# Optimization experiments

Measured on AMD Instinct MI355X. Metric: run time of the kernel, lower is better.

## Reference

```python
import jax, jax.numpy as jnp
import numpy as np

B, N, D = 4096, 64, 128
H, ATT = 8, 32
SCALE = ATT ** -0.5


def setup_inputs() -> dict:
    key = jax.random.key(0)
    k1, k2, k3, k4, k5 = jax.random.split(key, 5)
    x = jax.random.normal(k1, (B, N, D), dtype=jnp.float32)
    # glorot-ish scale for weights
    W_Q = jax.random.normal(k2, (H, D, ATT), dtype=jnp.float32) * (2.0 / (D + ATT)) ** 0.5
    W_K = jax.random.normal(k3, (H, D, ATT), dtype=jnp.float32) * (2.0 / (D + ATT)) ** 0.5
    W_V = jax.random.normal(k4, (H, D, ATT), dtype=jnp.float32) * (2.0 / (D + ATT)) ** 0.5
    W_res = jax.random.normal(k5, (D, H * ATT), dtype=jnp.float32) * (2.0 / (D + H * ATT)) ** 0.5
    return {"x": x, "W_Q": W_Q, "W_K": W_K, "W_V": W_V, "W_res": W_res}


def reference(x, W_Q, W_K, W_V, W_res):
    # per-head projections: (B,N,D) x (H,D,K) -> (B,H,N,K)
    Q = jnp.einsum('bnd,hdk->bhnk', x, W_Q)
    K = jnp.einsum('bnd,hdk->bhnk', x, W_K)
    V = jnp.einsum('bnd,hdk->bhnk', x, W_V)
    scores = jnp.einsum('bhnk,bhmk->bhnm', Q, K) * SCALE  # (B,H,N,N)
    attn = jax.nn.softmax(scores, axis=-1)
    ctx = jnp.einsum('bhnm,bhmk->bhnk', attn, V)          # (B,H,N,K)
    ctx = ctx.transpose(0, 2, 1, 3).reshape(x.shape[0], x.shape[1], H * ATT)
    res = x @ W_res  # d != H*att_dim -> residual projection
    return jax.nn.relu(ctx + res)
```

## Files before the change

### kernel.cpp

```cpp
#include <hip/hip_runtime.h>

#define NB    4096
#define SEQ   64
#define DIM   128
#define NHEAD 8
#define ATTD  32
#define HKC   256
#define SCALE 0.17677669529663687f
#define LOG2E 1.4426950408889634f

typedef __bf16 bf16_t;
typedef __bf16 bf16x8 __attribute__((ext_vector_type(8)));
typedef __bf16 bf16x4 __attribute__((ext_vector_type(4)));
typedef float  f32x4  __attribute__((ext_vector_type(4)));
typedef short  s16x4  __attribute__((ext_vector_type(4)));
typedef unsigned int u32;

#define MFMA16(a, b, c) __builtin_amdgcn_mfma_f32_16x16x16bf16_1k(a, b, c, 0, 0, 0)

static __device__ __forceinline__ u32 pkbf(float a, float b) {
  unsigned short ua = __builtin_bit_cast(unsigned short, (__bf16)a);
  unsigned short ub = __builtin_bit_cast(unsigned short, (__bf16)b);
  return (u32)ua | ((u32)ub << 16);
}

static __device__ __forceinline__ s16x4 pk4(f32x4 t) {
  union { u32 u[2]; s16x4 s; } r;
  r.u[0] = pkbf(t[0], t[1]);
  r.u[1] = pkbf(t[2], t[3]);
  return r.s;
}

#define XSWZ(r, c) (((r) << 7) + ((c) ^ (((r) & 7) << 3)))

__global__ void prep_weights(const float* __restrict__ Wq,
                             const float* __restrict__ Wk,
                             const float* __restrict__ Wv,
                             const float* __restrict__ Wr,
                             bf16_t* __restrict__ ws) {
  int idx = blockIdx.x * 256 + threadIdx.x;
  int m = idx >> 15;
  int e = idx & 32767;
  int c = e >> 7;
  int d = e & 127;
  float v;
  if (m == 0)      v = Wq[((c >> 5) * DIM + d) * ATTD + (c & 31)] * (SCALE * LOG2E);
  else if (m == 1) v = Wk[((c >> 5) * DIM + d) * ATTD + (c & 31)];
  else if (m == 2) v = Wv[((c >> 5) * DIM + d) * ATTD + (c & 31)];
  else             v = Wr[d * HKC + c];
  ws[idx] = (bf16_t)v;
}

__launch_bounds__(256, 3)
__global__ void fused_attn(const float* __restrict__ xg,
                           const bf16_t* __restrict__ ws,
                           float* __restrict__ outg) {
  __shared__ bf16_t Xb[64 * 128];

  const int t  = threadIdx.x;
  const int w  = t >> 6;
  const int l  = t & 63;
  const int lo = l & 15;
  const int g  = l >> 4;
  const int b  = blockIdx.x;

  {
    const float* xb = xg + (size_t)b * (SEQ * DIM);
#pragma unroll
    for (int i = 0; i < 8; ++i) {
      int idx = i * 1024 + t * 4;
      float4 v = *(const float4*)(xb + idx);
      bf16x4 p;
      p[0] = (bf16_t)v.x; p[1] = (bf16_t)v.y; p[2] = (bf16_t)v.z; p[3] = (bf16_t)v.w;
      *(bf16x4*)&Xb[XSWZ(idx >> 7, idx & 127)] = p;
    }
  }
  __syncthreads();

  const bf16_t* wsq = ws;
  const bf16_t* wsk = ws + 32768;
  const bf16_t* wsv = ws + 65536;
  const bf16_t* wsr = ws + 98304;
  float* ob = outg + (size_t)b * (SEQ * HKC);
  const f32x4 z4 = {0.f, 0.f, 0.f, 0.f};

#pragma unroll
  for (int hh = 0; hh < 2; ++hh) {
    const int hc = w * 64 + hh * 32;

    s16x4 kfr[2][4], vfr[4][2], qfr[2][4];

    {
      f32x4 acck[2][4];
#pragma unroll
      for (int i = 0; i < 2; ++i)
#pragma unroll
        for (int j = 0; j < 4; ++j) acck[i][j] = z4;
#pragma unroll
      for (int kk = 0; kk < 4; ++kk) {
        bf16x8 aw[2], bx[4];
#pragma unroll
        for (int at = 0; at < 2; ++at)
          aw[at] = *(const bf16x8*)(wsk + (hc + at * 16 + lo) * DIM + kk * 32 + g * 8);
#pragma unroll
        for (int nt = 0; nt < 4; ++nt)
          bx[nt] = *(const bf16x8*)&Xb[XSWZ(nt * 16 + lo, kk * 32 + g * 8)];
        __builtin_amdgcn_s_setprio(1);
#pragma unroll
        for (int at = 0; at < 2; ++at)
#pragma unroll
          for (int nt = 0; nt < 4; ++nt)
            acck[at][nt] = __builtin_amdgcn_mfma_f32_16x16x32_bf16(aw[at], bx[nt], acck[at][nt], 0, 0, 0);
        __builtin_amdgcn_s_setprio(0);
      }
#pragma unroll
      for (int at = 0; at < 2; ++at)
#pragma unroll
        for (int nt = 0; nt < 4; ++nt) kfr[at][nt] = pk4(acck[at][nt]);
    }

    {
      f32x4 accv[4][2];
#pragma unroll
      for (int i = 0; i < 4; ++i)
#pragma unroll
        for (int j = 0; j < 2; ++j) accv[i][j] = z4;
#pragma unroll
      for (int kk = 0; kk < 4; ++kk) {
        bf16x8 ax[4], bw[2];
#pragma unroll
        for (int nt = 0; nt < 4; ++nt)
          ax[nt] = *(const bf16x8*)&Xb[XSWZ(nt * 16 + lo, kk * 32 + g * 8)];
#pragma unroll
        for (int ct = 0; ct < 2; ++ct)
          bw[ct] = *(const bf16x8*)(wsv + (hc + ct * 16 + lo) * DIM + kk * 32 + g * 8);
        __builtin_amdgcn_s_setprio(1);
#pragma unroll
        for (int nt = 0; nt < 4; ++nt)
#pragma unroll
          for (int ct = 0; ct < 2; ++ct)
            accv[nt][ct] = __builtin_amdgcn_mfma_f32_16x16x32_bf16(ax[nt], bw[ct], accv[nt][ct], 0, 0, 0);
        __builtin_amdgcn_s_setprio(0);
      }
#pragma unroll
      for (int nt = 0; nt < 4; ++nt)
#pragma unroll
        for (int ct = 0; ct < 2; ++ct) vfr[nt][ct] = pk4(accv[nt][ct]);
    }

    {
      f32x4 accq[2][4];
#pragma unroll
      for (int i = 0; i < 2; ++i)
#pragma unroll
        for (int j = 0; j < 4; ++j) accq[i][j] = z4;
#pragma unroll
      for (int kk = 0; kk < 4; ++kk) {
        bf16x8 aw[2], bx[4];
#pragma unroll
        for (int at = 0; at < 2; ++at)
          aw[at] = *(const bf16x8*)(wsq + (hc + at * 16 + lo) * DIM + kk * 32 + g * 8);
#pragma unroll
        for (int mt = 0; mt < 4; ++mt)
          bx[mt] = *(const bf16x8*)&Xb[XSWZ(mt * 16 + lo, kk * 32 + g * 8)];
        __builtin_amdgcn_s_setprio(1);
#pragma unroll
        for (int at = 0; at < 2; ++at)
#pragma unroll
          for (int mt = 0; mt < 4; ++mt)
            accq[at][mt] = __builtin_amdgcn_mfma_f32_16x16x32_bf16(aw[at], bx[mt], accq[at][mt], 0, 0, 0);
        __builtin_amdgcn_s_setprio(0);
      }
#pragma unroll
      for (int at = 0; at < 2; ++at)
#pragma unroll
        for (int mt = 0; mt < 4; ++mt) qfr[at][mt] = pk4(accq[at][mt]);
    }

    f32x4 ch[2][4];
#pragma unroll
    for (int i = 0; i < 2; ++i)
#pragma unroll
      for (int j = 0; j < 4; ++j) ch[i][j] = z4;
#pragma unroll
    for (int mt = 0; mt < 4; ++mt) {
      f32x4 sv[4];
      __builtin_amdgcn_s_setprio(1);
#pragma unroll
      for (int nt = 0; nt < 4; ++nt)
        sv[nt] = MFMA16(kfr[0][nt], qfr[0][mt], z4);
#pragma unroll
      for (int nt = 0; nt < 4; ++nt)
        sv[nt] = MFMA16(kfr[1][nt], qfr[1][mt], sv[nt]);
      __builtin_amdgcn_s_setprio(0);
      bf16x8 bxr[4], awr[2];
#pragma unroll
      for (int mtj = 0; mtj < 4; ++mtj)
        bxr[mtj] = *(const bf16x8*)&Xb[XSWZ(mtj * 16 + lo, mt * 32 + g * 8)];
#pragma unroll
      for (int ct = 0; ct < 2; ++ct)
        awr[ct] = *(const bf16x8*)(wsr + (hc + ct * 16 + lo) * DIM + mt * 32 + g * 8);
      float ps[4];
#pragma unroll
      for (int nt = 0; nt < 4; ++nt) {
        float e0 = __builtin_amdgcn_exp2f(sv[nt][0]);
        float e1 = __builtin_amdgcn_exp2f(sv[nt][1]);
        float e2 = __builtin_amdgcn_exp2f(sv[nt][2]);
        float e3 = __builtin_amdgcn_exp2f(sv[nt][3]);
        sv[nt][0] = e0; sv[nt][1] = e1; sv[nt][2] = e2; sv[nt][3] = e3;
        ps[nt] = (e0 + e1) + (e2 + e3);
      }
      float sum = (ps[0] + ps[1]) + (ps[2] + ps[3]);
      s16x4 pfr[4];
#pragma unroll
      for (int nt = 0; nt < 4; ++nt) pfr[nt] = pk4(sv[nt]);
      __builtin_amdgcn_s_setprio(1);
#pragma unroll
      for (int ct = 0; ct < 2; ++ct)
#pragma unroll
        for (int mtj = 0; mtj < 4; ++mtj)
          ch[ct][mtj] = __builtin_amdgcn_mfma_f32_16x16x32_bf16(awr[ct], bxr[mtj], ch[ct][mtj], 0, 0, 0);
      __builtin_amdgcn_s_setprio(0);
      sum += __shfl_xor(sum, 16, 64);
      sum += __shfl_xor(sum, 32, 64);
      float rinv = __builtin_amdgcn_rcpf(sum);
      __builtin_amdgcn_s_setprio(1);
#pragma unroll
      for (int ct = 0; ct < 2; ++ct) {
        f32x4 a = MFMA16(vfr[0][ct], pfr[0], z4);
        a = MFMA16(vfr[1][ct], pfr[1], a);
        a = MFMA16(vfr[2][ct], pfr[2], a);
        a = MFMA16(vfr[3][ct], pfr[3], a);
#pragma unroll
        for (int j = 0; j < 4; ++j)
          ch[ct][mt][j] = fmaf(a[j], rinv, ch[ct][mt][j]);
      }
      __builtin_amdgcn_s_setprio(0);
    }

#pragma unroll
    for (int ct = 0; ct < 2; ++ct)
#pragma unroll
      for (int mt = 0; mt < 4; ++mt) {
        float4 o;
        o.x = fmaxf(ch[ct][mt][0], 0.f);
        o.y = fmaxf(ch[ct][mt][1], 0.f);
        o.z = fmaxf(ch[ct][mt][2], 0.f);
        o.w = fmaxf(ch[ct][mt][3], 0.f);
        *(float4*)(ob + (mt * 16 + lo) * HKC + hc + ct * 16 + 4 * g) = o;
      }
  }
}

extern "C" void kernel_launch(void* const* d_in, const int* in_sizes, int n_in,
                              void* d_out, int out_size, void* d_ws, size_t ws_size,
                              hipStream_t stream) {
  const float* x  = (const float*)d_in[0];
  const float* Wq = (const float*)d_in[1];
  const float* Wk = (const float*)d_in[2];
  const float* Wv = (const float*)d_in[3];
  const float* Wr = (const float*)d_in[4];
  bf16_t* ws = (bf16_t*)d_ws;
  float* out = (float*)d_out;

  prep_weights<<<512, 256, 0, stream>>>(Wq, Wk, Wv, Wr, ws);
  fused_attn<<<NB, 256, 0, stream>>>(x, ws, out);
}
```

Baseline: 178.3 us.

## Compute residual per query tile and store immediately to cut registers

The residual projection is restructured so each query tile computes its own 16-row residual block over the full K dimension, instead of accumulating all four tiles across the softmax loop. Each tile's output is written right after its attention step, so the eight persistent accumulators shrink to two. Launch bounds rise from 3 to 4 blocks per SIMD to use the freed registers for occupancy. The MFMA count is unchanged, but the global weight and LDS loads inside the loop are reorganized, and spills are possible if the new register cap is too tight.

```diff
diff --git a/kernel.cpp b/kernel.cpp
--- a/kernel.cpp
+++ b/kernel.cpp
@@ -51,7 +51,7 @@
   ws[idx] = (bf16_t)v;
 }
 
-__launch_bounds__(256, 3)
+__launch_bounds__(256, 4)
 __global__ void fused_attn(const float* __restrict__ xg,
                            const bf16_t* __restrict__ ws,
                            float* __restrict__ outg) {
@@ -177,11 +177,6 @@
         for (int mt = 0; mt < 4; ++mt) qfr[at][mt] = pk4(accq[at][mt]);
     }
 
-    f32x4 ch[2][4];
-#pragma unroll
-    for (int i = 0; i < 2; ++i)
-#pragma unroll
-      for (int j = 0; j < 4; ++j) ch[i][j] = z4;
 #pragma unroll
     for (int mt = 0; mt < 4; ++mt) {
       f32x4 sv[4];
@@ -193,13 +188,6 @@
       for (int nt = 0; nt < 4; ++nt)
         sv[nt] = MFMA16(kfr[1][nt], qfr[1][mt], sv[nt]);
       __builtin_amdgcn_s_setprio(0);
-      bf16x8 bxr[4], awr[2];
-#pragma unroll
-      for (int mtj = 0; mtj < 4; ++mtj)
-        bxr[mtj] = *(const bf16x8*)&Xb[XSWZ(mtj * 16 + lo, mt * 32 + g * 8)];
-#pragma unroll
-      for (int ct = 0; ct < 2; ++ct)
-        awr[ct] = *(const bf16x8*)(wsr + (hc + ct * 16 + lo) * DIM + mt * 32 + g * 8);
       float ps[4];
 #pragma unroll
       for (int nt = 0; nt < 4; ++nt) {
@@ -214,13 +202,17 @@
       s16x4 pfr[4];
 #pragma unroll
       for (int nt = 0; nt < 4; ++nt) pfr[nt] = pk4(sv[nt]);
-      __builtin_amdgcn_s_setprio(1);
-#pragma unroll
-      for (int ct = 0; ct < 2; ++ct)
-#pragma unroll
-        for (int mtj = 0; mtj < 4; ++mtj)
-          ch[ct][mtj] = __builtin_amdgcn_mfma_f32_16x16x32_bf16(awr[ct], bxr[mtj], ch[ct][mtj], 0, 0, 0);
-      __builtin_amdgcn_s_setprio(0);
+      f32x4 ch[2] = {z4, z4};
+#pragma unroll
+      for (int kk = 0; kk < 4; ++kk) {
+        bf16x8 bxr = *(const bf16x8*)&Xb[XSWZ(mt * 16 + lo, kk * 32 + g * 8)];
+        bf16x8 awr0 = *(const bf16x8*)(wsr + (hc + lo) * DIM + kk * 32 + g * 8);
+        bf16x8 awr1 = *(const bf16x8*)(wsr + (hc + 16 + lo) * DIM + kk * 32 + g * 8);
+        __builtin_amdgcn_s_setprio(1);
+        ch[0] = __builtin_amdgcn_mfma_f32_16x16x32_bf16(awr0, bxr, ch[0], 0, 0, 0);
+        ch[1] = __builtin_amdgcn_mfma_f32_16x16x32_bf16(awr1, bxr, ch[1], 0, 0, 0);
+        __builtin_amdgcn_s_setprio(0);
+      }
       sum += __shfl_xor(sum, 16, 64);
       sum += __shfl_xor(sum, 32, 64);
       float rinv = __builtin_amdgcn_rcpf(sum);
@@ -233,22 +225,19 @@
         a = MFMA16(vfr[3][ct], pfr[3], a);
 #pragma unroll
         for (int j = 0; j < 4; ++j)
-          ch[ct][mt][j] = fmaf(a[j], rinv, ch[ct][mt][j]);
+          ch[ct][j] = fmaf(a[j], rinv, ch[ct][j]);
       }
       __builtin_amdgcn_s_setprio(0);
-    }
-
-#pragma unroll
-    for (int ct = 0; ct < 2; ++ct)
-#pragma unroll
-      for (int mt = 0; mt < 4; ++mt) {
+#pragma unroll
+      for (int ct = 0; ct < 2; ++ct) {
         float4 o;
-        o.x = fmaxf(ch[ct][mt][0], 0.f);
-        o.y = fmaxf(ch[ct][mt][1], 0.f);
-        o.z = fmaxf(ch[ct][mt][2], 0.f);
-        o.w = fmaxf(ch[ct][mt][3], 0.f);
+        o.x = fmaxf(ch[ct][0], 0.f);
+        o.y = fmaxf(ch[ct][1], 0.f);
+        o.z = fmaxf(ch[ct][2], 0.f);
+        o.w = fmaxf(ch[ct][3], 0.f);
         *(float4*)(ob + (mt * 16 + lo) * HKC + hc + ct * 16 + 4 * g) = o;
       }
+    }
   }
 }
 
```

Result: slower. 247.6 us (+38.8%).
